# Performance work log

Measured on AMD Instinct MI355X. Metric: run time of the kernel, lower is better.

The kernel has to match this reference:

```python
import jax, jax.numpy as jnp
import numpy as np

N = 30000      # nodes
E = 480000     # edges per relation (avg degree 16)
H = 4          # GAT heads
D = 64         # out_size per head
F1, F2 = 256, 128   # per-metapath input feature dims
SIN = 256      # sen_in_size
HD = H * D     # 256, semantic-attention in_size
OUT = 64       # final out_size


def _gat(feat, src, dst, W, al, ar, b):
    """DGL GATConv (eval mode, dropout=0), activation=relu6."""
    h = (feat @ W).reshape(N, H, D)                     # [N,H,D]
    el = (h * al).sum(-1)                               # [N,H]
    er = (h * ar).sum(-1)                               # [N,H]
    e = jax.nn.leaky_relu(el[src] + er[dst], 0.2)       # [E,H]
    m = jax.ops.segment_max(e, dst, N)                  # edge-softmax over incoming edges
    p = jnp.exp(e - m[dst])
    s = jax.ops.segment_sum(p, dst, N)
    a = p / s[dst]                                      # [E,H]
    out = jax.ops.segment_sum(a[:, :, None] * h[src], dst, N)  # [N,H,D]
    out = out + b.reshape(1, H, D)
    return jnp.clip(out, 0.0, 6.0).reshape(N, H * D)    # relu6, flatten(1)


def _gcn_layer(x, src, dst, W, b):
    """DGL GraphConv, norm='both': D_in^{-1/2} A D_out^{-1/2} X W (+ b)."""
    ones = jnp.ones(src.shape[0], x.dtype)
    deg_o = jnp.clip(jax.ops.segment_sum(ones, src, N), 1.0, None)
    deg_i = jnp.clip(jax.ops.segment_sum(ones, dst, N), 1.0, None)
    h = (x @ W) * (deg_o[:, None] ** -0.5)
    h = jax.ops.segment_sum(h[src], dst, N) * (deg_i[:, None] ** -0.5)
    return h if b is None else h + b


def setup_inputs():
    key = jax.random.key(0)
    ks = jax.random.split(key, 28)
    f32 = jnp.float32
    nrm = lambda k, shp: jax.random.normal(k, shp, f32) * 0.05
    ri = lambda k, shp: jax.random.randint(k, shp, 0, N, jnp.int32)
    return dict(
        feat0=jax.random.normal(ks[0], (N, F1), f32),
        feat1=jax.random.normal(ks[1], (N, F2), f32),
        sen_feat=jax.random.normal(ks[2], (N, SIN), f32),
        Wgat0=nrm(ks[11], (F1, H * D)), al0=nrm(ks[12], (H, D)), ar0=nrm(ks[13], (H, D)), b0=nrm(ks[14], (H * D,)),
        Wgat1=nrm(ks[15], (F2, H * D)), al1=nrm(ks[16], (H, D)), ar1=nrm(ks[17], (H, D)), b1=nrm(ks[18], (H * D,)),
        Wp1=nrm(ks[19], (HD, OUT)), bp1=nrm(ks[20], (OUT,)), wp2=nrm(ks[21], (OUT,)),
        Wf=nrm(ks[22], (HD, OUT)), bf=nrm(ks[23], (OUT,)),
        Wg1=nrm(ks[24], (SIN, OUT)), bg1=nrm(ks[25], (OUT,)), Wg2=nrm(ks[26], (OUT, OUT)),
        src0=ri(ks[3], (E,)), dst0=ri(ks[4], (E,)),
        src1=ri(ks[5], (E,)), dst1=ri(ks[6], (E,)),
        gsrc=ri(ks[7], (E,)), gdst=ri(ks[8], (E,)),
        asrc=ri(ks[9], (E,)), adst=ri(ks[10], (E,)),
        k=10,
    )


def reference(feat0, feat1, sen_feat,
              Wgat0, al0, ar0, b0, Wgat1, al1, ar1, b1,
              Wp1, bp1, wp2, Wf, bf, Wg1, bg1, Wg2,
              src0, dst0, src1, dst1, gsrc, gdst, asrc, adst, k):
    # per-metapath GAT embeddings
    z0 = _gat(feat0, src0, dst0, Wgat0, al0, ar0, b0)   # [N, HD]
    z1 = _gat(feat1, src1, dst1, Wgat1, al1, ar1, b1)   # [N, HD]
    z = jnp.stack([z0, z1], axis=1)                     # [N, M=2, HD]
    # PathAttention (semantic attention over metapaths)
    w = jnp.tanh(z @ Wp1 + bp1) @ wp2                   # [N, M]
    beta = jax.nn.softmax(w.mean(0))                    # [M]
    fused = jnp.einsum('m,nmf->nf', beta, z)            # [N, HD]
    Femb = fused @ Wf + bf                              # [N, OUT]
    # two-layer GCN on the sentence graph
    p1 = jnp.tanh(_gcn_layer(sen_feat, gsrc, gdst, Wg1, bg1))
    P = _gcn_layer(p1, gsrc, gdst, Wg2, None)           # [N, OUT]
    # spectral loss: fuse embeddings, trace of Laplacian quadratic form on first k dims
    Z = 0.5 * (Femb + P)                                # [N, OUT]
    Zk = Z[:, :k]
    diff = Zk[asrc] - Zk[adst]
    tr = 0.5 * jnp.sum(diff * diff)                     # tr(Zk^T (D - A) Zk)
    return (tr, Z)
```

## Files before the change

### kernel.cpp

```cpp
#include <hip/hip_runtime.h>
#include <math.h>

#define NN 30000
#define NE 480000
#define NBLK 118
#define NMT 235
#define NTRB 7500

typedef unsigned short ushort_t;
typedef unsigned int uint_t;
typedef __attribute__((ext_vector_type(8))) short short8;
typedef __attribute__((ext_vector_type(4))) float f32x4;

__device__ __forceinline__ ushort_t f2bf(float x) {
  uint_t u = __float_as_uint(x);
  u = (u + 0x7FFF + ((u >> 16) & 1)) >> 16;
  return (ushort_t)u;
}
__device__ __forceinline__ float bf2f(ushort_t v) {
  return __uint_as_float(((uint_t)v) << 16);
}

__device__ __forceinline__ float wred(float v) {
#pragma unroll
  for (int off = 32; off > 0; off >>= 1) v += __shfl_xor(v, off);
  return v;
}

__global__ void prep_kernel(float4* __restrict__ zp, const float* __restrict__ W0,
                            const float* __restrict__ W1, const float* __restrict__ W2,
                            const float* __restrict__ W3, const float* __restrict__ W4,
                            ushort_t* __restrict__ T0, ushort_t* __restrict__ T1,
                            ushort_t* __restrict__ T2, ushort_t* __restrict__ T3,
                            ushort_t* __restrict__ T4, const float* __restrict__ F0,
                            const float* __restrict__ F1, ushort_t* __restrict__ B0,
                            ushort_t* __restrict__ B1) {
  int id = blockIdx.x * 256 + threadIdx.x;
  if (id < 52501) {
    zp[id] = make_float4(0.f, 0.f, 0.f, 0.f);
    return;
  }
  int wid = id - 52501;
  if (wid < 147456) {
    const float* W;
    ushort_t* T;
    int K, N, base;
    if (wid < 65536) { W = W0; T = T0; K = 256; N = 256; base = 0; }
    else if (wid < 98304) { W = W1; T = T1; K = 128; N = 256; base = 65536; }
    else if (wid < 114688) { W = W2; T = T2; K = 256; N = 64; base = 98304; }
    else if (wid < 131072) { W = W3; T = T3; K = 256; N = 64; base = 114688; }
    else { W = W4; T = T4; K = 256; N = 64; base = 131072; }
    int l = wid - base;
    int k = l / N, n = l - k * N;
    T[(size_t)n * K + k] = f2bf(W[l]);
    return;
  }
  int cid = wid - 147456;
  const float* S;
  ushort_t* D;
  if (cid < 960000) { S = F0; D = B0; }
  else {
    cid -= 960000;
    if (cid >= 480000) return;
    S = F1; D = B1;
  }
  const float4* p = (const float4*)(S + (size_t)cid * 8);
  float4 a = p[0], b = p[1];
  short8 o;
  o[0] = (short)f2bf(a.x); o[1] = (short)f2bf(a.y);
  o[2] = (short)f2bf(a.z); o[3] = (short)f2bf(a.w);
  o[4] = (short)f2bf(b.x); o[5] = (short)f2bf(b.y);
  o[6] = (short)f2bf(b.z); o[7] = (short)f2bf(b.w);
  *(short8*)(D + (size_t)cid * 8) = o;
}


__device__ __forceinline__ void mfma_core_f32(const float* __restrict__ A0,
                                              const ushort_t* __restrict__ BT, int K, int bm,
                                              short* __restrict__ As, short* __restrict__ Bs,
                                              f32x4 acc[2][4]) {
  int tid = threadIdx.x;
  int lane = tid & 63, w = tid >> 6;
  int q = lane >> 4, mr = lane & 15;
#pragma unroll 1
  for (int k0 = 0; k0 < K; k0 += 32) {
    {
      int r = tid >> 1, hf = tid & 1;
      int gr = bm + r;
      float4 f0 = make_float4(0.f, 0.f, 0.f, 0.f), f1 = f0, f2 = f0, f3 = f0;
      if (gr < NN) {
        const float4* pa = (const float4*)(A0 + (size_t)gr * K + k0 + hf * 16);
        f0 = pa[0]; f1 = pa[1]; f2 = pa[2]; f3 = pa[3];
      }
      short8 lo, hi;
      lo[0] = (short)f2bf(f0.x); lo[1] = (short)f2bf(f0.y);
      lo[2] = (short)f2bf(f0.z); lo[3] = (short)f2bf(f0.w);
      lo[4] = (short)f2bf(f1.x); lo[5] = (short)f2bf(f1.y);
      lo[6] = (short)f2bf(f1.z); lo[7] = (short)f2bf(f1.w);
      hi[0] = (short)f2bf(f2.x); hi[1] = (short)f2bf(f2.y);
      hi[2] = (short)f2bf(f2.z); hi[3] = (short)f2bf(f2.w);
      hi[4] = (short)f2bf(f3.x); hi[5] = (short)f2bf(f3.y);
      hi[6] = (short)f2bf(f3.z); hi[7] = (short)f2bf(f3.w);
      short* dst = As + r * 40 + hf * 16;
      *(short8*)(dst) = lo;
      *(short8*)(dst + 8) = hi;
    }
    {
      int n = tid >> 2, qk = tid & 3;
      short8 bv = *(const short8*)((const short*)BT + (size_t)n * K + k0 + qk * 8);
      *(short8*)(Bs + n * 40 + qk * 8) = bv;
    }
    __syncthreads();
    short8 a0 = *(short8*)(As + (w * 32 + mr) * 40 + q * 8);
    short8 a1 = *(short8*)(As + (w * 32 + 16 + mr) * 40 + q * 8);
#pragma unroll
    for (int j = 0; j < 4; ++j) {
      short8 b = *(short8*)(Bs + (j * 16 + mr) * 40 + q * 8);
      acc[0][j] = __builtin_amdgcn_mfma_f32_16x16x32_bf16(a0, b, acc[0][j], 0, 0, 0);
      acc[1][j] = __builtin_amdgcn_mfma_f32_16x16x32_bf16(a1, b, acc[1][j], 0, 0, 0);
    }
    __syncthreads();
  }
}

__device__ __forceinline__ void mfma_core2_bfK(const ushort_t* __restrict__ A0,
                                               const ushort_t* __restrict__ BT, int K, int bm,
                                               short* __restrict__ As, short* __restrict__ Bs,
                                               f32x4 acc[2][8]) {
  int tid = threadIdx.x;
  int lane = tid & 63, w = tid >> 6;
  int q = lane >> 4, mr = lane & 15;
#pragma unroll 1
  for (int k0 = 0; k0 < K; k0 += 32) {
    {
      int r = tid >> 1, hf = tid & 1;
      int gr = bm + r;
      short8 v0 = {0, 0, 0, 0, 0, 0, 0, 0}, v1 = v0;
      if (gr < NN) {
        const short* p0 = (const short*)A0 + (size_t)gr * K + k0 + hf * 16;
        v0 = *(const short8*)p0;
        v1 = *(const short8*)(p0 + 8);
      }
      short* dst = As + r * 40 + hf * 16;
      *(short8*)(dst) = v0;
      *(short8*)(dst + 8) = v1;
    }
    {
      int n = tid >> 1, qk = tid & 1;
      const short* src = (const short*)BT + (size_t)n * K + k0 + qk * 16;
      short8 b0 = *(const short8*)src;
      short8 b1 = *(const short8*)(src + 8);
      short* d = Bs + n * 40 + qk * 16;
      *(short8*)d = b0;
      *(short8*)(d + 8) = b1;
    }
    __syncthreads();
    short8 a0 = *(short8*)(As + (w * 32 + mr) * 40 + q * 8);
    short8 a1 = *(short8*)(As + (w * 32 + 16 + mr) * 40 + q * 8);
#pragma unroll
    for (int j = 0; j < 8; ++j) {
      short8 b = *(short8*)(Bs + (j * 16 + mr) * 40 + q * 8);
      acc[0][j] = __builtin_amdgcn_mfma_f32_16x16x32_bf16(a0, b, acc[0][j], 0, 0, 0);
      acc[1][j] = __builtin_amdgcn_mfma_f32_16x16x32_bf16(a1, b, acc[1][j], 0, 0, 0);
    }
    __syncthreads();
  }
}

__global__ __launch_bounds__(256) void mfma_all_kernel(
    const ushort_t* __restrict__ fB0, const ushort_t* __restrict__ fB1,
    const float* __restrict__ sen, const ushort_t* __restrict__ WT0,
    const ushort_t* __restrict__ WT1, const ushort_t* __restrict__ Wg1T,
    ushort_t* __restrict__ h0, ushort_t* __restrict__ h1, ushort_t* __restrict__ gcnA,
    const float* __restrict__ al0, const float* __restrict__ ar0, float* __restrict__ el0,
    float* __restrict__ er0, const float* __restrict__ al1, const float* __restrict__ ar1,
    float* __restrict__ el1, float* __restrict__ er1, const float* __restrict__ rdo) {
  __shared__ short As[128 * 40];
  __shared__ short Bs[128 * 40];
  int y = blockIdx.y;
  int bm = blockIdx.x * 128;
  int lane = threadIdx.x & 63, w = threadIdx.x >> 6;
  int q = lane >> 4, mr = lane & 15;
  if (y < 4) {
    int gsel = y >> 1, p = y & 1;
    const ushort_t* A = gsel ? fB1 : fB0;
    int K = gsel ? 128 : 256;
    const ushort_t* WT = gsel ? WT1 : WT0;
    ushort_t* H = gsel ? h1 : h0;
    const float* al = gsel ? al1 : al0;
    const float* ar = gsel ? ar1 : ar0;
    float* el = gsel ? el1 : el0;
    float* er = gsel ? er1 : er0;
    f32x4 acc[2][8];
#pragma unroll
    for (int i = 0; i < 2; ++i)
#pragma unroll
      for (int j = 0; j < 8; ++j) acc[i][j] = (f32x4){0.f, 0.f, 0.f, 0.f};
    mfma_core2_bfK(A, WT + (size_t)p * 128 * K, K, bm, As, Bs, acc);
    float alv[8], arv[8];
#pragma unroll
    for (int j = 0; j < 8; ++j) {
      alv[j] = al[p * 128 + j * 16 + mr];
      arv[j] = ar[p * 128 + j * 16 + mr];
    }
#pragma unroll
    for (int i = 0; i < 2; ++i)
#pragma unroll
      for (int r = 0; r < 4; ++r) {
        int gr = bm + w * 32 + i * 16 + q * 4 + r;
        float pl0 = 0.f, pr0 = 0.f, pl1 = 0.f, pr1 = 0.f;
#pragma unroll
        for (int j = 0; j < 4; ++j) {
          pl0 = fmaf(acc[i][j][r], alv[j], pl0);
          pr0 = fmaf(acc[i][j][r], arv[j], pr0);
          pl1 = fmaf(acc[i][j + 4][r], alv[j + 4], pl1);
          pr1 = fmaf(acc[i][j + 4][r], arv[j + 4], pr1);
        }
#pragma unroll
        for (int m = 1; m < 16; m <<= 1) {
          pl0 += __shfl_xor(pl0, m);
          pr0 += __shfl_xor(pr0, m);
          pl1 += __shfl_xor(pl1, m);
          pr1 += __shfl_xor(pr1, m);
        }
        if (gr < NN) {
          if (mr == 0) {
            el[gr * 4 + 2 * p] = pl0;
            er[gr * 4 + 2 * p] = pr0;
            el[gr * 4 + 2 * p + 1] = pl1;
            er[gr * 4 + 2 * p + 1] = pr1;
          }
#pragma unroll
          for (int j = 0; j < 8; ++j)
            H[(size_t)gr * 256 + p * 128 + j * 16 + mr] = f2bf(acc[i][j][r]);
        }
      }
  } else {
    f32x4 acc[2][4];
#pragma unroll
    for (int i = 0; i < 2; ++i)
#pragma unroll
      for (int j = 0; j < 4; ++j) acc[i][j] = (f32x4){0.f, 0.f, 0.f, 0.f};
    mfma_core_f32(sen, Wg1T, 256, bm, As, Bs, acc);
#pragma unroll
    for (int i = 0; i < 2; ++i)
#pragma unroll
      for (int r = 0; r < 4; ++r) {
        int gr = bm + w * 32 + i * 16 + q * 4 + r;
        if (gr < NN) {
          float sc = rdo[gr];
#pragma unroll
          for (int j = 0; j < 4; ++j)
            gcnA[(size_t)gr * 64 + j * 16 + mr] = f2bf(acc[i][j][r] * sc);
        }
      }
  }
}

__global__ __launch_bounds__(256) void mfma_attnwf_kernel(
    const ushort_t* __restrict__ z0, const ushort_t* __restrict__ z1,
    const ushort_t* __restrict__ WpfT, const float* __restrict__ bp1,
    const float* __restrict__ wp2, float* __restrict__ pbuf, ushort_t* __restrict__ Y0,
    ushort_t* __restrict__ Y1) {
  __shared__ short As[128 * 40];
  __shared__ short Bs[128 * 40];
  __shared__ float wsum[4];
  const ushort_t* A = blockIdx.y ? z1 : z0;
  ushort_t* Y = blockIdx.y ? Y1 : Y0;
  int bm = blockIdx.x * 128;
  f32x4 acc[2][8];
#pragma unroll
  for (int i = 0; i < 2; ++i)
#pragma unroll
    for (int j = 0; j < 8; ++j) acc[i][j] = (f32x4){0.f, 0.f, 0.f, 0.f};
  mfma_core2_bfK(A, WpfT, 256, bm, As, Bs, acc);
  int lane = threadIdx.x & 63, w = threadIdx.x >> 6;
  int q = lane >> 4, mr = lane & 15;
  float local = 0.f;
#pragma unroll
  for (int j = 0; j < 4; ++j) {
    int col = j * 16 + mr;
    float bp = bp1[col], wp = wp2[col];
#pragma unroll
    for (int i = 0; i < 2; ++i)
#pragma unroll
      for (int r = 0; r < 4; ++r) {
        int gr = bm + w * 32 + i * 16 + q * 4 + r;
        if (gr < NN) local += tanhf(acc[i][j][r] + bp) * wp;
      }
  }
  local = wred(local);
  if (lane == 0) wsum[w] = local;
#pragma unroll
  for (int j = 4; j < 8; ++j) {
    int col = (j - 4) * 16 + mr;
#pragma unroll
    for (int i = 0; i < 2; ++i)
#pragma unroll
      for (int r = 0; r < 4; ++r) {
        int gr = bm + w * 32 + i * 16 + q * 4 + r;
        if (gr < NN) Y[(size_t)gr * 64 + col] = f2bf(acc[i][j][r]);
      }
  }
  __syncthreads();
  if (threadIdx.x == 0)
    pbuf[blockIdx.y * NMT + blockIdx.x] = wsum[0] + wsum[1] + wsum[2] + wsum[3];
}

__global__ void hist_kernel(const int* __restrict__ d0, const int* __restrict__ d1,
                            const int* __restrict__ d2, const int* __restrict__ d3,
                            int* __restrict__ cnt) {
  int g = blockIdx.y;
  const int* d = g == 0 ? d0 : g == 1 ? d1 : g == 2 ? d2 : d3;
  int e = blockIdx.x * 256 + threadIdx.x;
  if (e < NE) atomicAdd(&cnt[g * NN + d[e]], 1);
}

__global__ __launch_bounds__(256) void scan_blocks_kernel(const int* __restrict__ cnt,
                                                          int* __restrict__ rows,
                                                          int* __restrict__ bsum) {
  __shared__ int sm[256];
  int g = blockIdx.y, t = threadIdx.x;
  int i = blockIdx.x * 256 + t;
  int v = (i < NN) ? cnt[g * NN + i] : 0;
  sm[t] = v;
  __syncthreads();
#pragma unroll
  for (int off = 1; off < 256; off <<= 1) {
    int tmp = (t >= off) ? sm[t - off] : 0;
    __syncthreads();
    sm[t] += tmp;
    __syncthreads();
  }
  if (i < NN) rows[g * (NN + 1) + i] = sm[t] - v;
  if (t == 255) bsum[g * NBLK + blockIdx.x] = sm[255];
}

__global__ __launch_bounds__(128) void scan_tops_kernel(int* __restrict__ bsum,
                                                        int* __restrict__ boff) {
  __shared__ int sm[128];
  int g = blockIdx.y, t = threadIdx.x;
  int v = (t < NBLK) ? bsum[g * NBLK + t] : 0;
  sm[t] = v;
  __syncthreads();
#pragma unroll
  for (int off = 1; off < 128; off <<= 1) {
    int tmp = (t >= off) ? sm[t - off] : 0;
    __syncthreads();
    sm[t] += tmp;
    __syncthreads();
  }
  if (t < NBLK) boff[g * NBLK + t] = sm[t] - v;
}

__global__ void add_off_kernel(int* __restrict__ rows, const int* __restrict__ boff) {
  int g = blockIdx.y, t = threadIdx.x;
  int i = blockIdx.x * 256 + t;
  if (i < NN) rows[g * (NN + 1) + i] += boff[g * NBLK + blockIdx.x];
  if (blockIdx.x == 0 && t == 0) rows[g * (NN + 1) + NN] = NE;
}

__global__ void scatter_kernel(const int* __restrict__ s0, const int* __restrict__ s1,
                               const int* __restrict__ s2, const int* __restrict__ d0,
                               const int* __restrict__ d1, const int* __restrict__ d2,
                               const int* __restrict__ rows, int* __restrict__ cnt2,
                               int* __restrict__ cols, const int* __restrict__ cnt_deg,
                               float* __restrict__ rdo, float* __restrict__ rdi,
                               const int* __restrict__ rows_g) {
  int g = blockIdx.y;
  if (g == 3) {
    int n = blockIdx.x * 256 + threadIdx.x;
    if (n < NN) {
      rdo[n] = rsqrtf(fmaxf((float)cnt_deg[n], 1.f));
      float di = (float)(rows_g[n + 1] - rows_g[n]);
      rdi[n] = rsqrtf(fmaxf(di, 1.f));
    }
    return;
  }
  const int* sp = g == 0 ? s0 : g == 1 ? s1 : s2;
  const int* dp = g == 0 ? d0 : g == 1 ? d1 : d2;
  int e = blockIdx.x * 256 + threadIdx.x;
  if (e >= NE) return;
  int d = dp[e];
  int pos = rows[g * (NN + 1) + d] + atomicAdd(&cnt2[g * NN + d], 1);
  cols[(size_t)g * NE + pos] = sp[e];
}

__global__ __launch_bounds__(256) void sort_kernel(const int* __restrict__ rows0,
                                                   int* __restrict__ cols0,
                                                   const int* __restrict__ rows1,
                                                   int* __restrict__ cols1) {
  int g = blockIdx.y;
  const int* rows = g ? rows1 : rows0;
  int* cols = g ? cols1 : cols0;
  int lane = threadIdx.x & 63, w = threadIdx.x >> 6;
  int half = lane >> 5, ll = lane & 31;
  int n = blockIdx.x * 8 + w * 2 + half;
  if (n >= NN) return;
  int r0 = rows[n], r1 = rows[n + 1];
  int deg = r1 - r0;
  if (deg < 2 || deg > 32) return;
  int v = (ll < deg) ? cols[r0 + ll] : 0x7FFFFFFF;
#pragma unroll
  for (int k = 2; k <= 32; k <<= 1) {
#pragma unroll
    for (int j = k >> 1; j > 0; j >>= 1) {
      int o = __shfl_xor(v, j);
      bool up = ((ll & k) == 0);
      bool lower = ((ll & j) == 0);
      int mn = v < o ? v : o;
      int mx = v < o ? o : v;
      v = (up == lower) ? mn : mx;
    }
  }
  if (ll < deg) cols[r0 + ll] = v;
}

__global__ __launch_bounds__(256) void gat_node_kernel(
    const int* __restrict__ rows0, const int* __restrict__ cols0, const float* __restrict__ el0,
    const float* __restrict__ er0, const ushort_t* __restrict__ h0,
    const float* __restrict__ bias0, ushort_t* __restrict__ zz0, const int* __restrict__ rows1,
    const int* __restrict__ cols1, const float* __restrict__ el1, const float* __restrict__ er1,
    const ushort_t* __restrict__ h1, const float* __restrict__ bias1,
    ushort_t* __restrict__ zz1) {
  int g = blockIdx.y;
  const int* rows = g ? rows1 : rows0;
  const int* cols = g ? cols1 : cols0;
  const float* el = g ? el1 : el0;
  const float* er = g ? er1 : er0;
  const ushort_t* h = g ? h1 : h0;
  const float* bias = g ? bias1 : bias0;
  ushort_t* z = g ? zz1 : zz0;

  int lane = threadIdx.x & 63, w = threadIdx.x >> 6;
  int n = blockIdx.x * 4 + w;
  int hh = lane >> 4;
  float4 er4 = *(const float4*)&er[n * 4];
  float myer = hh == 0 ? er4.x : hh == 1 ? er4.y : hh == 2 ? er4.z : er4.w;
  int r0 = rows[n], r1 = rows[n + 1];
  int deg = r1 - r0;
  float ssum = 0.f;
  float4 acc = make_float4(0.f, 0.f, 0.f, 0.f);
  for (int j = 0; j < deg; j += 16) {
    int si[16];
#pragma unroll
    for (int t = 0; t < 16; ++t) {
      int jj = j + t;
      int jx = jj < deg ? jj : deg - 1;
      si[t] = cols[r0 + jx];
    }
    float ev[16];
#pragma unroll
    for (int t = 0; t < 16; ++t) ev[t] = el[si[t] * 4 + hh];
    ushort4 hv[16];
#pragma unroll
    for (int t = 0; t < 16; ++t) hv[t] = *(const ushort4*)&h[(size_t)si[t] * 256 + lane * 4];
#pragma unroll
    for (int t = 0; t < 16; ++t) {
      float v = ev[t] + myer;
      v = v > 0.f ? v : 0.2f * v;
      float e = __expf(v);
      e = (j + t < deg) ? e : 0.f;
      ssum += e;
      acc.x = fmaf(e, bf2f(hv[t].x), acc.x);
      acc.y = fmaf(e, bf2f(hv[t].y), acc.y);
      acc.z = fmaf(e, bf2f(hv[t].z), acc.z);
      acc.w = fmaf(e, bf2f(hv[t].w), acc.w);
    }
  }
  float invd = (deg > 0) ? 1.f / ssum : 0.f;
  float4 bv = *(const float4*)&bias[lane * 4];
  ushort4 o;
  o.x = f2bf(fminf(fmaxf(acc.x * invd + bv.x, 0.f), 6.f));
  o.y = f2bf(fminf(fmaxf(acc.y * invd + bv.y, 0.f), 6.f));
  o.z = f2bf(fminf(fmaxf(acc.z * invd + bv.z, 0.f), 6.f));
  o.w = f2bf(fminf(fmaxf(acc.w * invd + bv.w, 0.f), 6.f));
  *(ushort4*)&z[(size_t)n * 256 + lane * 4] = o;
}

__global__ __launch_bounds__(256) void gcn_gather12_kernel(
    const int* __restrict__ rows, const int* __restrict__ cols, const ushort_t* __restrict__ X,
    const float* __restrict__ rdi, const float* __restrict__ bg1, const float* __restrict__ Wg2,
    const float* __restrict__ rdo, ushort_t* __restrict__ out2, const float* __restrict__ pbuf,
    float* __restrict__ wb) {
  __shared__ float psm[4][64];
  int lane = threadIdx.x & 63, w = threadIdx.x >> 6;
  if (blockIdx.x == 0) {
    __shared__ float sm[8];
    int t = threadIdx.x;
    float a0 = 0.f, a1 = 0.f;
    for (int i = t; i < NMT; i += 256) {
      a0 += pbuf[i];
      a1 += pbuf[NMT + i];
    }
    a0 = wred(a0);
    a1 = wred(a1);
    if (lane == 0) { sm[w] = a0; sm[4 + w] = a1; }
    __syncthreads();
    if (t == 0) {
      float w0 = (sm[0] + sm[1] + sm[2] + sm[3]) * (1.0f / NN);
      float w1 = (sm[4] + sm[5] + sm[6] + sm[7]) * (1.0f / NN);
      float mx = fmaxf(w0, w1);
      float e0 = expf(w0 - mx), e1 = expf(w1 - mx);
      float inv = 1.f / (e0 + e1);
      wb[2] = e0 * inv;
      wb[3] = e1 * inv;
    }
  }
  int n = blockIdx.x * 4 + w;
  if (n >= NN) return;
  int r0 = rows[n], r1 = rows[n + 1];
  int eg = lane >> 4, fl = lane & 15;
  float facc[4] = {0.f, 0.f, 0.f, 0.f};
  for (int j = r0; j < r1; j += 16) {
    int si[4];
    float sel[4];
#pragma unroll
    for (int t = 0; t < 4; ++t) {
      int jj = j + 4 * t + eg;
      int jx = jj < r1 ? jj : r1 - 1;
      si[t] = cols[jx];
      sel[t] = (jj < r1) ? 1.f : 0.f;
    }
    ushort4 xv[4];
#pragma unroll
    for (int t = 0; t < 4; ++t) xv[t] = *(const ushort4*)&X[(size_t)si[t] * 64 + fl * 4];
#pragma unroll
    for (int t = 0; t < 4; ++t) {
      facc[0] = fmaf(sel[t], bf2f(xv[t].x), facc[0]);
      facc[1] = fmaf(sel[t], bf2f(xv[t].y), facc[1]);
      facc[2] = fmaf(sel[t], bf2f(xv[t].z), facc[2]);
      facc[3] = fmaf(sel[t], bf2f(xv[t].w), facc[3]);
    }
  }
#pragma unroll
  for (int u = 0; u < 4; ++u) {
    facc[u] += __shfl_xor(facc[u], 16);
    facc[u] += __shfl_xor(facc[u], 32);
  }
  if (eg == 0) *(float4*)&psm[w][fl * 4] = make_float4(facc[0], facc[1], facc[2], facc[3]);
  __syncthreads();
  float p = tanhf(psm[w][lane] * rdi[n] + bg1[lane]);
  float o = 0.f;
#pragma unroll
  for (int k = 0; k < 64; ++k) o = fmaf(__shfl(p, k), Wg2[k * 64 + lane], o);
  out2[(size_t)n * 64 + lane] = f2bf(o * rdo[n]);
}

__global__ __launch_bounds__(256) void gcn_gather2_kernel(
    const int* __restrict__ rows, const int* __restrict__ cols, const ushort_t* __restrict__ X,
    const float* __restrict__ rdi, const ushort_t* __restrict__ Y0,
    const ushort_t* __restrict__ Y1, const float* __restrict__ wb, const float* __restrict__ bf,
    const int* __restrict__ kptr, float* __restrict__ Zc, float* __restrict__ dout) {
  int lane = threadIdx.x & 63, w = threadIdx.x >> 6;
  int n = blockIdx.x * 4 + w;
  if (n >= NN) return;
  int r0 = rows[n], r1 = rows[n + 1];
  int eg = lane >> 4, fl = lane & 15;
  float facc[4] = {0.f, 0.f, 0.f, 0.f};
  for (int j = r0; j < r1; j += 16) {
    int si[4];
    float sel[4];
#pragma unroll
    for (int t = 0; t < 4; ++t) {
      int jj = j + 4 * t + eg;
      int jx = jj < r1 ? jj : r1 - 1;
      si[t] = cols[jx];
      sel[t] = (jj < r1) ? 1.f : 0.f;
    }
    ushort4 xv[4];
#pragma unroll
    for (int t = 0; t < 4; ++t) xv[t] = *(const ushort4*)&X[(size_t)si[t] * 64 + fl * 4];
#pragma unroll
    for (int t = 0; t < 4; ++t) {
      facc[0] = fmaf(sel[t], bf2f(xv[t].x), facc[0]);
      facc[1] = fmaf(sel[t], bf2f(xv[t].y), facc[1]);
      facc[2] = fmaf(sel[t], bf2f(xv[t].z), facc[2]);
      facc[3] = fmaf(sel[t], bf2f(xv[t].w), facc[3]);
    }
  }
#pragma unroll
  for (int u = 0; u < 4; ++u) {
    facc[u] += __shfl_xor(facc[u], 16);
    facc[u] += __shfl_xor(facc[u], 32);
  }
  if (eg == 0) {
    float ri = rdi[n];
    ushort4 y0 = *(const ushort4*)&Y0[(size_t)n * 64 + fl * 4];
    ushort4 y1 = *(const ushort4*)&Y1[(size_t)n * 64 + fl * 4];
    float4 bfv = *(const float4*)&bf[fl * 4];
    float w2 = wb[2], w3 = wb[3];
    float zv[4];
    zv[0] = 0.5f * (w2 * bf2f(y0.x) + w3 * bf2f(y1.x) + bfv.x + facc[0] * ri);
    zv[1] = 0.5f * (w2 * bf2f(y0.y) + w3 * bf2f(y1.y) + bfv.y + facc[1] * ri);
    zv[2] = 0.5f * (w2 * bf2f(y0.z) + w3 * bf2f(y1.z) + bfv.z + facc[2] * ri);
    zv[3] = 0.5f * (w2 * bf2f(y0.w) + w3 * bf2f(y1.w) + bfv.w + facc[3] * ri);
    float* dp = dout + 1 + (size_t)n * 64 + fl * 4;
    dp[0] = zv[0]; dp[1] = zv[1]; dp[2] = zv[2]; dp[3] = zv[3];
    int k = *kptr;
    if (fl < 4) {
      float4 zk;
      zk.x = (fl * 4 + 0 < k) ? zv[0] : 0.f;
      zk.y = (fl * 4 + 1 < k) ? zv[1] : 0.f;
      zk.z = (fl * 4 + 2 < k) ? zv[2] : 0.f;
      zk.w = (fl * 4 + 3 < k) ? zv[3] : 0.f;
      *(float4*)&Zc[(size_t)n * 16 + fl * 4] = zk;
    }
  }
}

__global__ __launch_bounds__(256) void tr_kernel(const int* __restrict__ asrc,
                                                 const int* __restrict__ adst,
                                                 const int* __restrict__ kptr,
                                                 const float* __restrict__ Zc,
                                                 const float* __restrict__ dout,
                                                 float* __restrict__ trbuf) {
  __shared__ float wsum[4];
  int lane = threadIdx.x & 63, w = threadIdx.x >> 6;
  int k = *kptr;
  int eg = lane >> 2, c0 = (lane & 3) * 4;
  int e = blockIdx.x * 64 + w * 16 + eg;
  float local = 0.f;
  if (e < NE) {
    int a = asrc[e], b = adst[e];
    if (k <= 16) {
      float4 za = *(const float4*)&Zc[(size_t)a * 16 + c0];
      float4 zb = *(const float4*)&Zc[(size_t)b * 16 + c0];
      float dx = za.x - zb.x, dy = za.y - zb.y, dz = za.z - zb.z, dw = za.w - zb.w;
      local = dx * dx + dy * dy + dz * dz + dw * dw;
    } else {
      const float* Za = dout + 1 + (size_t)a * 64;
      const float* Zb = dout + 1 + (size_t)b * 64;
#pragma unroll
      for (int st = 0; st < 4; ++st) {
#pragma unroll
        for (int t = 0; t < 4; ++t) {
          int c = c0 + st * 16 + t;
          if (c < k) {
            float d2 = Za[c] - Zb[c];
            local += d2 * d2;
          }
        }
      }
    }
  }
#pragma unroll
  for (int off = 32; off > 0; off >>= 1) local += __shfl_down(local, off);
  if (lane == 0) wsum[w] = local;
  __syncthreads();
  if (threadIdx.x == 0) trbuf[blockIdx.x] = wsum[0] + wsum[1] + wsum[2] + wsum[3];
}

__global__ __launch_bounds__(256) void tr_reduce_kernel(const float* __restrict__ trbuf,
                                                        float* __restrict__ dout) {
  __shared__ float sm[4];
  int t = threadIdx.x;
  float a = 0.f;
  for (int i = t; i < NTRB; i += 256) a += trbuf[i];
  a = wred(a);
  int lane = t & 63, w = t >> 6;
  if (lane == 0) sm[w] = a;
  __syncthreads();
  if (t == 0) dout[0] = 0.5f * (sm[0] + sm[1] + sm[2] + sm[3]);
}

extern "C" void kernel_launch(void* const* d_in, const int* in_sizes, int n_in, void* d_out,
                              int out_size, void* d_ws, size_t ws_size, hipStream_t stream) {
  const float* feat0 = (const float*)d_in[0];
  const float* feat1 = (const float*)d_in[1];
  const float* sen = (const float*)d_in[2];
  const float* Wgat0 = (const float*)d_in[3];
  const float* al0 = (const float*)d_in[4];
  const float* ar0 = (const float*)d_in[5];
  const float* b0 = (const float*)d_in[6];
  const float* Wgat1 = (const float*)d_in[7];
  const float* al1 = (const float*)d_in[8];
  const float* ar1 = (const float*)d_in[9];
  const float* b1 = (const float*)d_in[10];
  const float* Wp1 = (const float*)d_in[11];
  const float* bp1 = (const float*)d_in[12];
  const float* wp2 = (const float*)d_in[13];
  const float* Wf = (const float*)d_in[14];
  const float* bf = (const float*)d_in[15];
  const float* Wg1 = (const float*)d_in[16];
  const float* bg1 = (const float*)d_in[17];
  const float* Wg2 = (const float*)d_in[18];
  const int* src0 = (const int*)d_in[19];
  const int* dst0 = (const int*)d_in[20];
  const int* src1 = (const int*)d_in[21];
  const int* dst1 = (const int*)d_in[22];
  const int* gsrc = (const int*)d_in[23];
  const int* gdst = (const int*)d_in[24];
  const int* asrc = (const int*)d_in[25];
  const int* adst = (const int*)d_in[26];
  const int* kptr = (const int*)d_in[27];
  float* out = (float*)d_out;
  float* ws = (float*)d_ws;

  float* wb = ws;
  int* cnt = (int*)(ws + 4);
  int* cnt2 = (int*)(ws + 120004);
  float* rdo = ws + 210004;
  float* rdi = ws + 240004;
  int* rows = (int*)(ws + 270004);
  int* bsum = (int*)(ws + 360008);
  int* boff = (int*)(ws + 360364);
  int* cols = (int*)(ws + 360720);
  float* el0 = ws + 1800720;
  float* er0 = ws + 1920720;
  float* el1 = ws + 2040720;
  float* er1 = ws + 2160720;
  float* pbuf = ws + 2280720;
  float* trbuf = el0;
  ushort_t* h0 = (ushort_t*)(ws + 2283068);
  ushort_t* h1 = (ushort_t*)(ws + 6123068);
  ushort_t* z0 = (ushort_t*)(ws + 9963068);
  ushort_t* z1 = (ushort_t*)(ws + 13803068);
  ushort_t* gcnA = (ushort_t*)(ws + 17643068);
  ushort_t* gcnA2 = (ushort_t*)(ws + 18603068);
  ushort_t* Y0 = (ushort_t*)(ws + 19563068);
  ushort_t* Y1 = (ushort_t*)(ws + 20523068);
  ushort_t* WT0 = (ushort_t*)(ws + 21483068);
  ushort_t* WT1 = (ushort_t*)(ws + 21515836);
  ushort_t* WpfT = (ushort_t*)(ws + 21532220);
  ushort_t* Wg1T = (ushort_t*)(ws + 21548604);
  float* Zc = ws + 21556796;

  int* rows_g = rows + 2 * (NN + 1);
  int* cols_g = cols + 2 * NE;
  int* cnt_deg = cnt + 3 * NN;

  ushort_t* fB0 = z0;
  ushort_t* fB1 = z1;

  prep_kernel<<<6407, 256, 0, stream>>>((float4*)ws, Wgat0, Wgat1, Wp1, Wf, Wg1, WT0, WT1, WpfT,
                                        WpfT + 16384, Wg1T, feat0, feat1, fB0, fB1);

  hist_kernel<<<dim3(1875, 4), 256, 0, stream>>>(dst0, dst1, gdst, gsrc, cnt);
  scan_blocks_kernel<<<dim3(NBLK, 3), 256, 0, stream>>>(cnt, rows, bsum);
  scan_tops_kernel<<<dim3(1, 3), 128, 0, stream>>>(bsum, boff);
  add_off_kernel<<<dim3(NBLK, 3), 256, 0, stream>>>(rows, boff);
  scatter_kernel<<<dim3(1875, 4), 256, 0, stream>>>(src0, src1, gsrc, dst0, dst1, gdst, rows,
                                                    cnt2, cols, cnt_deg, rdo, rdi, rows_g);

  sort_kernel<<<dim3(3750, 2), 256, 0, stream>>>(rows, cols, rows + (NN + 1), cols + NE);

  mfma_all_kernel<<<dim3(NMT, 5), 256, 0, stream>>>(fB0, fB1, sen, WT0, WT1, Wg1T, h0, h1,
                                                    gcnA, al0, ar0, el0, er0, al1, ar1, el1,
                                                    er1, rdo);

  gat_node_kernel<<<dim3(7500, 2), 256, 0, stream>>>(rows, cols, el0, er0, h0, b0, z0,
                                                     rows + (NN + 1), cols + NE, el1, er1, h1,
                                                     b1, z1);

  mfma_attnwf_kernel<<<dim3(NMT, 2), 256, 0, stream>>>(z0, z1, WpfT, bp1, wp2, pbuf, Y0, Y1);

  gcn_gather12_kernel<<<7500, 256, 0, stream>>>(rows_g, cols_g, gcnA, rdi, bg1, Wg2, rdo, gcnA2,
                                                pbuf, wb);
  gcn_gather2_kernel<<<7500, 256, 0, stream>>>(rows_g, cols_g, gcnA2, rdi, Y0, Y1, wb, bf, kptr,
                                               Zc, out);

  tr_kernel<<<NTRB, 256, 0, stream>>>(asrc, adst, kptr, Zc, out, trbuf);
  tr_reduce_kernel<<<1, 256, 0, stream>>>(trbuf, out);
}
```

Measured before the change: 529.3 us.

## Precompute GAT edge weights in shared memory and drop the per-node column sort

The GAT aggregation kernel now computes the edge exponentials for all four heads once per edge, with edges spread across lanes, stores them in shared memory (up to a cap of 128 edges per node), and wave-reduces the softmax denominators. This replaces the redundant per-lane recomputation of leaky-relu and exp in the gather loop. Edges past the cap are handled by a slower fallback loop. The bitonic sort of CSR columns is removed, which drops a kernel launch but leaves the neighbour order and the floating-point summation order nondeterministic, and may reduce locality in the h gathers.

Measured after the change: 515.7 us (median of 2 runs). 1.03x faster.

```diff
diff --git a/kernel.cpp b/kernel.cpp
--- a/kernel.cpp
+++ b/kernel.cpp
@@ -6,6 +6,7 @@
 #define NBLK 118
 #define NMT 235
 #define NTRB 7500
+#define CAPD 128
 
 typedef unsigned short ushort_t;
 typedef unsigned int uint_t;
@@ -386,36 +387,6 @@
   cols[(size_t)g * NE + pos] = sp[e];
 }
 
-__global__ __launch_bounds__(256) void sort_kernel(const int* __restrict__ rows0,
-                                                   int* __restrict__ cols0,
-                                                   const int* __restrict__ rows1,
-                                                   int* __restrict__ cols1) {
-  int g = blockIdx.y;
-  const int* rows = g ? rows1 : rows0;
-  int* cols = g ? cols1 : cols0;
-  int lane = threadIdx.x & 63, w = threadIdx.x >> 6;
-  int half = lane >> 5, ll = lane & 31;
-  int n = blockIdx.x * 8 + w * 2 + half;
-  if (n >= NN) return;
-  int r0 = rows[n], r1 = rows[n + 1];
-  int deg = r1 - r0;
-  if (deg < 2 || deg > 32) return;
-  int v = (ll < deg) ? cols[r0 + ll] : 0x7FFFFFFF;
-#pragma unroll
-  for (int k = 2; k <= 32; k <<= 1) {
-#pragma unroll
-    for (int j = k >> 1; j > 0; j >>= 1) {
-      int o = __shfl_xor(v, j);
-      bool up = ((ll & k) == 0);
-      bool lower = ((ll & j) == 0);
-      int mn = v < o ? v : o;
-      int mx = v < o ? o : v;
-      v = (up == lower) ? mn : mx;
-    }
-  }
-  if (ll < deg) cols[r0 + ll] = v;
-}
-
 __global__ __launch_bounds__(256) void gat_node_kernel(
     const int* __restrict__ rows0, const int* __restrict__ cols0, const float* __restrict__ el0,
     const float* __restrict__ er0, const ushort_t* __restrict__ h0,
@@ -423,6 +394,7 @@
     const int* __restrict__ cols1, const float* __restrict__ el1, const float* __restrict__ er1,
     const ushort_t* __restrict__ h1, const float* __restrict__ bias1,
     ushort_t* __restrict__ zz1) {
+  __shared__ float aw[4][CAPD][4];
   int g = blockIdx.y;
   const int* rows = g ? rows1 : rows0;
   const int* cols = g ? cols1 : cols0;
@@ -434,41 +406,63 @@
 
   int lane = threadIdx.x & 63, w = threadIdx.x >> 6;
   int n = blockIdx.x * 4 + w;
-  int hh = lane >> 4;
-  float4 er4 = *(const float4*)&er[n * 4];
-  float myer = hh == 0 ? er4.x : hh == 1 ? er4.y : hh == 2 ? er4.z : er4.w;
   int r0 = rows[n], r1 = rows[n + 1];
   int deg = r1 - r0;
-  float ssum = 0.f;
+  float4 er4 = *(const float4*)&er[n * 4];
+  float s0 = 0.f, s1 = 0.f, s2 = 0.f, s3 = 0.f;
+  for (int j = lane; j < deg; j += 64) {
+    int s = cols[r0 + j];
+    float4 elv = *(const float4*)&el[s * 4];
+    float v0 = elv.x + er4.x; v0 = v0 > 0.f ? v0 : 0.2f * v0;
+    float v1 = elv.y + er4.y; v1 = v1 > 0.f ? v1 : 0.2f * v1;
+    float v2 = elv.z + er4.z; v2 = v2 > 0.f ? v2 : 0.2f * v2;
+    float v3 = elv.w + er4.w; v3 = v3 > 0.f ? v3 : 0.2f * v3;
+    float e0 = __expf(v0), e1 = __expf(v1), e2 = __expf(v2), e3 = __expf(v3);
+    s0 += e0; s1 += e1; s2 += e2; s3 += e3;
+    if (j < CAPD) {
+      aw[w][j][0] = e0; aw[w][j][1] = e1; aw[w][j][2] = e2; aw[w][j][3] = e3;
+    }
+  }
+  s0 = wred(s0); s1 = wred(s1); s2 = wred(s2); s3 = wred(s3);
+  __syncthreads();
+  int hh = lane >> 4;
+  float denom = hh == 0 ? s0 : hh == 1 ? s1 : hh == 2 ? s2 : s3;
+  float myer = hh == 0 ? er4.x : hh == 1 ? er4.y : hh == 2 ? er4.z : er4.w;
+  float invd = (deg > 0) ? 1.f / denom : 0.f;
   float4 acc = make_float4(0.f, 0.f, 0.f, 0.f);
-  for (int j = 0; j < deg; j += 16) {
+  int jc = deg < CAPD ? deg : CAPD;
+  for (int j = 0; j < jc; j += 16) {
     int si[16];
+    float ai[16];
 #pragma unroll
     for (int t = 0; t < 16; ++t) {
       int jj = j + t;
-      int jx = jj < deg ? jj : deg - 1;
+      int jx = jj < jc ? jj : jc - 1;
       si[t] = cols[r0 + jx];
-    }
-    float ev[16];
-#pragma unroll
-    for (int t = 0; t < 16; ++t) ev[t] = el[si[t] * 4 + hh];
-    ushort4 hv[16];
-#pragma unroll
-    for (int t = 0; t < 16; ++t) hv[t] = *(const ushort4*)&h[(size_t)si[t] * 256 + lane * 4];
+      ai[t] = (jj < jc) ? aw[w][jj][hh] : 0.f;
+    }
+    ushort4 ui[16];
+#pragma unroll
+    for (int t = 0; t < 16; ++t) ui[t] = *(const ushort4*)&h[(size_t)si[t] * 256 + lane * 4];
 #pragma unroll
     for (int t = 0; t < 16; ++t) {
-      float v = ev[t] + myer;
-      v = v > 0.f ? v : 0.2f * v;
-      float e = __expf(v);
-      e = (j + t < deg) ? e : 0.f;
-      ssum += e;
-      acc.x = fmaf(e, bf2f(hv[t].x), acc.x);
-      acc.y = fmaf(e, bf2f(hv[t].y), acc.y);
-      acc.z = fmaf(e, bf2f(hv[t].z), acc.z);
-      acc.w = fmaf(e, bf2f(hv[t].w), acc.w);
-    }
-  }
-  float invd = (deg > 0) ? 1.f / ssum : 0.f;
+      acc.x = fmaf(ai[t], bf2f(ui[t].x), acc.x);
+      acc.y = fmaf(ai[t], bf2f(ui[t].y), acc.y);
+      acc.z = fmaf(ai[t], bf2f(ui[t].z), acc.z);
+      acc.w = fmaf(ai[t], bf2f(ui[t].w), acc.w);
+    }
+  }
+  for (int j = jc; j < deg; ++j) {
+    int s = cols[r0 + j];
+    float v = el[s * 4 + hh] + myer;
+    v = v > 0.f ? v : 0.2f * v;
+    float a = __expf(v);
+    ushort4 hu = *(const ushort4*)&h[(size_t)s * 256 + lane * 4];
+    acc.x = fmaf(a, bf2f(hu.x), acc.x);
+    acc.y = fmaf(a, bf2f(hu.y), acc.y);
+    acc.z = fmaf(a, bf2f(hu.z), acc.z);
+    acc.w = fmaf(a, bf2f(hu.w), acc.w);
+  }
   float4 bv = *(const float4*)&bias[lane * 4];
   ushort4 o;
   o.x = f2bf(fminf(fmaxf(acc.x * invd + bv.x, 0.f), 6.f));
@@ -743,8 +737,6 @@
   scatter_kernel<<<dim3(1875, 4), 256, 0, stream>>>(src0, src1, gsrc, dst0, dst1, gdst, rows,
                                                     cnt2, cols, cnt_deg, rdo, rdi, rows_g);
 
-  sort_kernel<<<dim3(3750, 2), 256, 0, stream>>>(rows, cols, rows + (NN + 1), cols + NE);
-
   mfma_all_kernel<<<dim3(NMT, 5), 256, 0, stream>>>(fB0, fB1, sen, WT0, WT1, Wg1T, h0, h1,
                                                     gcnA, al0, ar0, el0, er0, al1, ar1, el1,
                                                     er1, rdo);
```
